# Kernel tuning notes

Hardware: AMD Instinct MI355X
Metric: run time of the kernel (lower is better)

Reference implementation:

```python
import jax, jax.numpy as jnp
import numpy as np

B, T, C, H = 2, 2048, 2048, 16
D = C // H  # head_dim = 128
SCALE = 1.0 / np.sqrt(D)


def setup_inputs() -> dict:
    key = jax.random.key(0)
    ks = jax.random.split(key, 9)
    x = jax.random.normal(ks[0], (B, T, C), dtype=jnp.float32)
    # additive causal mask [T, T]
    attn_mask = jnp.where(jnp.tril(jnp.ones((T, T), dtype=bool)), 0.0, -1e9).astype(jnp.float32)
    s_cc = 1.0 / np.sqrt(C)
    s_cd = 1.0 / np.sqrt(C)
    Wq = jax.random.normal(ks[1], (C, C), dtype=jnp.float32) * s_cc
    Wk = jax.random.normal(ks[2], (D, C), dtype=jnp.float32) * s_cd
    Wv = jax.random.normal(ks[3], (D, C), dtype=jnp.float32) * s_cd
    Wo = jax.random.normal(ks[4], (C, C), dtype=jnp.float32) * s_cc
    bq = jnp.zeros((C,), jnp.float32)
    bk = jnp.zeros((D,), jnp.float32)
    bv = jnp.zeros((D,), jnp.float32)
    bo = jnp.zeros((C,), jnp.float32)
    return {"x": x, "attn_mask": attn_mask, "Wq": Wq, "bq": bq, "Wk": Wk,
            "bk": bk, "Wv": Wv, "bv": bv, "Wo": Wo, "bo": bo}


def reference(x, attn_mask, Wq, bq, Wk, bk, Wv, bv, Wo, bo):
    # projections (torch Linear: x @ W.T + b)
    q = (x @ Wq.T + bq).reshape(B, T, H, D).transpose(0, 2, 1, 3)  # [B,H,T,D]
    k = x @ Wk.T + bk                                              # [B,T,D] single KV head
    v = x @ Wv.T + bv                                              # [B,T,D]
    # scores: broadcast shared K over all H query heads
    scores = jnp.einsum('bhtd,bsd->bhts', q, k) * SCALE            # [B,H,T,T]
    scores = scores + attn_mask  # [T,T] broadcasts over B,H
    attn = jax.nn.softmax(scores, axis=-1)
    out = jnp.einsum('bhts,bsd->bhtd', attn, v)                    # [B,H,T,D]
    out = out.transpose(0, 2, 1, 3).reshape(B, T, C)
    return out @ Wo.T + bo
```

## Files before the change

kernel.cpp:

```cpp
#include <hip/hip_runtime.h>
#include <stdint.h>

typedef unsigned short u16;
typedef __attribute__((ext_vector_type(8))) __bf16 bf16x8;
typedef __attribute__((ext_vector_type(4))) float f32x4;
typedef __attribute__((ext_vector_type(8))) u16 u16x8;

#define B_SZ 2
#define T_SZ 2048
#define C_SZ 2048
#define H_SZ 16
#define D_SZ 128
#define NQKV 2304
#define ATT_SCALE 0.08838834764831845f

typedef __attribute__((address_space(1))) void* as1_void_p;
typedef __attribute__((address_space(3))) void* as3_void_p;

__device__ __forceinline__ u16 f2b(float f) {
  union { float f; uint32_t u; } c; c.f = f;
  return (u16)((c.u + 0x7FFFu + ((c.u >> 16) & 1u)) >> 16);
}

__device__ __forceinline__ void gload_lds16(const u16* g, u16* l) {
  __builtin_amdgcn_global_load_lds((as1_void_p)g, (as3_void_p)l, 16, 0, 0);
}

__global__ __launch_bounds__(256) void cast_to_bf16(const float* __restrict__ in,
                                                    u16* __restrict__ out, int n) {
  int idx = (blockIdx.x * 256 + threadIdx.x) * 4;
  if (idx >= n) return;
  float4 f = *(const float4*)&in[idx];
  ushort4 o4;
  o4.x = f2b(f.x); o4.y = f2b(f.y); o4.z = f2b(f.z); o4.w = f2b(f.w);
  *(ushort4*)&out[idx] = o4;
}

__global__ __launch_bounds__(256) void build_bias(const float* __restrict__ bq,
                                                  const float* __restrict__ bk,
                                                  const float* __restrict__ bv,
                                                  float* __restrict__ out) {
  int i = blockIdx.x * 256 + threadIdx.x;
  if (i < C_SZ) out[i] = bq[i];
  else if (i < C_SZ + D_SZ) out[i] = bk[i - C_SZ];
  else if (i < NQKV) out[i] = bv[i - C_SZ - D_SZ];
}

template <typename OutT>
__global__ __launch_bounds__(256) void gemm_bt(const u16* __restrict__ A,
                                               const u16* __restrict__ Bm,
                                               const float* __restrict__ bias,
                                               OutT* __restrict__ C,
                                               int K, int ldc) {
  __shared__ u16 lsA[128 * 32];
  __shared__ u16 lsB[128 * 32];
  const int tid = threadIdx.x;
  const int lane = tid & 63;
  const int wave = tid >> 6;
  const int wr = wave >> 1, wc = wave & 1;
  const int l16 = lane & 15, lq = lane >> 4;
  const int brow = blockIdx.y * 128;
  const int bcol = blockIdx.x * 128;

  f32x4 acc[4][4] = {};

  for (int k0 = 0; k0 < K; k0 += 32) {
    __syncthreads();
#pragma unroll
    for (int i = 0; i < 2; i++) {
      const int woff = (i * 4 + wave) * 512;
      const int eoff = woff + lane * 8;
      const int r = eoff >> 5, c = eoff & 31;
      gload_lds16(A + (size_t)(brow + r) * K + k0 + c, &lsA[woff]);
      gload_lds16(Bm + (size_t)(bcol + r) * K + k0 + c, &lsB[woff]);
    }
    __syncthreads();

    bf16x8 af[4], bfr[4];
#pragma unroll
    for (int mi = 0; mi < 4; mi++)
      af[mi] = *(const bf16x8*)&lsA[(wr * 64 + mi * 16 + l16) * 32 + lq * 8];
#pragma unroll
    for (int ni = 0; ni < 4; ni++)
      bfr[ni] = *(const bf16x8*)&lsB[(wc * 64 + ni * 16 + l16) * 32 + lq * 8];
#pragma unroll
    for (int mi = 0; mi < 4; mi++)
#pragma unroll
      for (int ni = 0; ni < 4; ni++)
        acc[mi][ni] = __builtin_amdgcn_mfma_f32_16x16x32_bf16(af[mi], bfr[ni], acc[mi][ni], 0, 0, 0);
  }

#pragma unroll
  for (int mi = 0; mi < 4; mi++)
#pragma unroll
    for (int ni = 0; ni < 4; ni++) {
      const int col = bcol + wc * 64 + ni * 16 + l16;
      const float bb = bias ? bias[col] : 0.0f;
#pragma unroll
      for (int r = 0; r < 4; r++) {
        const int row = brow + wr * 64 + mi * 16 + lq * 4 + r;
        const float v = acc[mi][ni][r] + bb;
        if constexpr (sizeof(OutT) == 2) {
          ((u16*)C)[(size_t)row * ldc + col] = f2b(v);
        } else {
          ((float*)C)[(size_t)row * ldc + col] = v;
        }
      }
    }
}

__global__ __launch_bounds__(256) void transpose_v(const u16* __restrict__ qkv,
                                                   u16* __restrict__ vT) {
  __shared__ u16 tile[64 * 136];
  const int tid = threadIdx.x;
  const int t0 = blockIdx.x * 64;
  const int b = blockIdx.y;
#pragma unroll
  for (int i = 0; i < 4; i++) {
    int idx = (i * 256 + tid) * 8;
    int r = idx >> 7, c = idx & 127;
    u16x8 v = *(const u16x8*)&qkv[(size_t)(b * T_SZ + t0 + r) * NQKV + (C_SZ + D_SZ) + c];
    *(u16x8*)&tile[r * 136 + c] = v;
  }
  __syncthreads();
#pragma unroll
  for (int i = 0; i < 4; i++) {
    int idx = (i * 256 + tid) * 8;
    int d = idx >> 6, t = idx & 63;
    u16x8 v;
#pragma unroll
    for (int j = 0; j < 8; j++) v[j] = tile[(t + j) * 136 + d];
    *(u16x8*)&vT[(size_t)(b * D_SZ + d) * T_SZ + t0 + t] = v;
  }
}

__device__ __forceinline__ void attn_tile(
    const u16* lk, const u16* lv, u16* lsPw,
    const bf16x8 (&aq)[4], f32x4 (&o)[8], float (&mrow)[4], float (&lrow)[4],
    int relrow, int l16, int lq)
{
  f32x4 s[4] = {};
#pragma unroll
  for (int kk = 0; kk < 4; kk++) {
#pragma unroll
    for (int nb = 0; nb < 4; nb++) {
      const int row = nb * 16 + l16;
      const bf16x8 bk = *(const bf16x8*)&lk[row * 128 + (((kk * 4 + lq) ^ (row & 7)) << 3)];
      s[nb] = __builtin_amdgcn_mfma_f32_16x16x32_bf16(aq[kk], bk, s[nb], 0, 0, 0);
    }
  }
#pragma unroll
  for (int rr = 0; rr < 4; rr++) {
    const int rowrel = relrow + lq * 4 + rr;
    float mx = -3.0e38f;
#pragma unroll
    for (int nb = 0; nb < 4; nb++) {
      float xv = s[nb][rr] * ATT_SCALE;
      if (nb * 16 + l16 > rowrel) xv -= 1e9f;
      s[nb][rr] = xv;
      mx = fmaxf(mx, xv);
    }
#pragma unroll
    for (int sh = 8; sh >= 1; sh >>= 1) mx = fmaxf(mx, __shfl_xor(mx, sh, 64));
    const float mnew = fmaxf(mrow[rr], mx);
    const float alpha = __expf(mrow[rr] - mnew);
    mrow[rr] = mnew;
    float rs = 0.f;
#pragma unroll
    for (int nb = 0; nb < 4; nb++) {
      const float p = __expf(s[nb][rr] - mnew);
      s[nb][rr] = p;
      rs += p;
    }
#pragma unroll
    for (int sh = 8; sh >= 1; sh >>= 1) rs += __shfl_xor(rs, sh, 64);
    lrow[rr] = lrow[rr] * alpha + rs;
#pragma unroll
    for (int nd = 0; nd < 8; nd++) o[nd][rr] *= alpha;
  }
  __builtin_amdgcn_sched_barrier(0);
#pragma unroll
  for (int nb = 0; nb < 4; nb++)
#pragma unroll
    for (int rr = 0; rr < 4; rr++) {
      const int qr = lq * 4 + rr;
      const int col = nb * 16 + l16;
      lsPw[qr * 64 + ((((col >> 3) ^ (qr & 7)) << 3) | (col & 7))] = f2b(s[nb][rr]);
    }
  asm volatile("s_waitcnt lgkmcnt(0)" ::: "memory");
  __builtin_amdgcn_sched_barrier(0);
#pragma unroll
  for (int ks = 0; ks < 2; ks++) {
    const bf16x8 pa = *(const bf16x8*)&lsPw[l16 * 64 + (((ks * 4 + lq) ^ (l16 & 7)) << 3)];
#pragma unroll
    for (int nd = 0; nd < 8; nd++) {
      const int row = nd * 16 + l16;
      const bf16x8 bv = *(const bf16x8*)&lv[row * 64 + (((ks * 4 + lq) ^ (row & 7)) << 3)];
      o[nd] = __builtin_amdgcn_mfma_f32_16x16x32_bf16(pa, bv, o[nd], 0, 0, 0);
    }
  }
}

__global__ __launch_bounds__(256, 2) void attn_fwd(const u16* __restrict__ qkv,
                                                   const u16* __restrict__ vT,
                                                   u16* __restrict__ out) {
  __shared__ u16 lsK[2][64 * 128];
  __shared__ u16 lsV[2][128 * 64];
  __shared__ u16 lsP[4][16 * 64];
  const int tid = threadIdx.x;
  const int w = tid >> 6, lane = tid & 63;
  const int l16 = lane & 15, lq = lane >> 4;
  const int qL = blockIdx.x;
  const int qH = 31 - qL;
  const int h = blockIdx.y;
  const int b = blockIdx.z;
  const int bT = b * T_SZ;

  bf16x8 aqL[4], aqH[4];
  {
    const size_t rL = (size_t)(bT + qL * 64 + w * 16 + l16) * NQKV + h * D_SZ;
    const size_t rH = (size_t)(bT + qH * 64 + w * 16 + l16) * NQKV + h * D_SZ;
#pragma unroll
    for (int kk = 0; kk < 4; kk++) {
      aqL[kk] = *(const bf16x8*)&qkv[rL + kk * 32 + lq * 8];
      aqH[kk] = *(const bf16x8*)&qkv[rH + kk * 32 + lq * 8];
    }
  }

  f32x4 oL[8] = {}, oH[8] = {};
  float mL[4] = {-INFINITY, -INFINITY, -INFINITY, -INFINITY};
  float mH[4] = {-INFINITY, -INFINITY, -INFINITY, -INFINITY};
  float lL[4] = {0.f, 0.f, 0.f, 0.f};
  float lH[4] = {0.f, 0.f, 0.f, 0.f};

  auto STAGE = [&](int kt, int bufsel) {
    const int kv0 = kt << 6;
#pragma unroll
    for (int j = 0; j < 4; j++) {
      const int idx = w * 256 + j * 64 + lane;
      const int row = idx >> 4, c = idx & 15;
      const int sc = c ^ (row & 7);
      gload_lds16(qkv + (size_t)(bT + kv0 + row) * NQKV + C_SZ + sc * 8,
                  &lsK[bufsel][w * 2048 + j * 512]);
    }
#pragma unroll
    for (int j = 0; j < 4; j++) {
      const int idx = w * 256 + j * 64 + lane;
      const int row = idx >> 3, c = idx & 7;
      const int sc = c ^ (row & 7);
      gload_lds16(vT + (size_t)(b * D_SZ + row) * T_SZ + kv0 + sc * 8,
                  &lsV[bufsel][w * 2048 + j * 512]);
    }
  };

  STAGE(0, 0);
  __syncthreads();
  int cur = 0;
  for (int kt = 0; kt <= qH; kt++) {
    if (kt < qH) STAGE(kt + 1, cur ^ 1);
    attn_tile(lsK[cur], lsV[cur], lsP[w], aqH, oH, mH, lH,
              (qH - kt) * 64 + w * 16, l16, lq);
    if (kt <= qL)
      attn_tile(lsK[cur], lsV[cur], lsP[w], aqL, oL, mL, lL,
                (qL - kt) * 64 + w * 16, l16, lq);
    __syncthreads();
    cur ^= 1;
  }

#pragma unroll
  for (int nd = 0; nd < 8; nd++)
#pragma unroll
    for (int rr = 0; rr < 4; rr++) {
      const int rL_ = qL * 64 + w * 16 + lq * 4 + rr;
      const int rH_ = qH * 64 + w * 16 + lq * 4 + rr;
      out[(size_t)(bT + rL_) * C_SZ + h * D_SZ + nd * 16 + l16] = f2b(oL[nd][rr] / lL[rr]);
      out[(size_t)(bT + rH_) * C_SZ + h * D_SZ + nd * 16 + l16] = f2b(oH[nd][rr] / lH[rr]);
    }
}

extern "C" void kernel_launch(void* const* d_in, const int* in_sizes, int n_in,
                              void* d_out, int out_size, void* d_ws, size_t ws_size,
                              hipStream_t stream) {
  const float* x  = (const float*)d_in[0];
  const float* Wq = (const float*)d_in[2];
  const float* bq = (const float*)d_in[3];
  const float* Wk = (const float*)d_in[4];
  const float* bk = (const float*)d_in[5];
  const float* Wv = (const float*)d_in[6];
  const float* bv = (const float*)d_in[7];
  const float* Wo = (const float*)d_in[8];
  const float* bo = (const float*)d_in[9];
  float* out = (float*)d_out;

  char* ws = (char*)d_ws;
  if (ws_size < 71312384) return;
  u16* xb     = (u16*)(ws + 0);
  u16* wqkv   = (u16*)(ws + 16777216);
  u16* wob    = (u16*)(ws + 26214400);
  u16* qkv    = (u16*)(ws + 34603008);
  u16* vT     = (u16*)(ws + 53477376);
  u16* ao     = (u16*)(ws + 54525952);
  float* bqkv = (float*)(ws + 71303168);

  cast_to_bf16<<<8192, 256, 0, stream>>>(x, xb, 8388608);
  cast_to_bf16<<<4096, 256, 0, stream>>>(Wq, wqkv, 4194304);
  cast_to_bf16<<<256, 256, 0, stream>>>(Wk, wqkv + 4194304, 262144);
  cast_to_bf16<<<256, 256, 0, stream>>>(Wv, wqkv + 4456448, 262144);
  cast_to_bf16<<<4096, 256, 0, stream>>>(Wo, wob, 4194304);
  build_bias<<<9, 256, 0, stream>>>(bq, bk, bv, bqkv);

  gemm_bt<u16><<<dim3(18, 32), 256, 0, stream>>>(xb, wqkv, bqkv, qkv, 2048, NQKV);
  transpose_v<<<dim3(32, 2), 256, 0, stream>>>(qkv, vT);
  attn_fwd<<<dim3(16, 16, 2), 256, 0, stream>>>(qkv, vT, ao);
  gemm_bt<float><<<dim3(16, 32), 256, 0, stream>>>(ao, wob, bo, out, 2048, 2048);
}
```

Measured before the change: 245.5 us.

## Restructure attention into 32-key tiles with lazy softmax rescale and causal skipping

The attention kernel drops the paired low/high query-tile scheme and launches one block per 64-row query tile, heaviest first. K/V tiles shrink to 32 keys, so LDS use is smaller and occupancy can rise (launch bounds raised to 4 blocks per CU). Each warp skips key tiles entirely above its own 16 query rows and applies the causal mask only on diagonal tiles. Softmax now uses one running max per warp group that is updated only when it grows past a threshold (FA4-style deferred rescale), scale is folded into exp, and row-sum reductions move to the epilogue. The risks are more load imbalance without pairing, and precision issues from the shared, lagging max.

Result: slower. 277.9 us (+13.2%).

```diff
diff --git a/kernel.cpp b/kernel.cpp
--- a/kernel.cpp
+++ b/kernel.cpp
@@ -13,6 +13,7 @@
 #define D_SZ 128
 #define NQKV 2304
 #define ATT_SCALE 0.08838834764831845f
+#define DEFER_THR 90.50967f
 
 typedef __attribute__((address_space(1))) void* as1_void_p;
 typedef __attribute__((address_space(3))) void* as3_void_p;
@@ -134,147 +135,144 @@
   }
 }
 
-__device__ __forceinline__ void attn_tile(
+template <bool MASK>
+__device__ __forceinline__ void attn_tile32(
     const u16* lk, const u16* lv, u16* lsPw,
-    const bf16x8 (&aq)[4], f32x4 (&o)[8], float (&mrow)[4], float (&lrow)[4],
-    int relrow, int l16, int lq)
+    const bf16x8 (&aq)[4], f32x4 (&o)[8], float (&lp)[4], float& mgrp,
+    int relq, int l16, int lq)
 {
-  f32x4 s[4] = {};
+  f32x4 s[2] = {};
 #pragma unroll
   for (int kk = 0; kk < 4; kk++) {
 #pragma unroll
-    for (int nb = 0; nb < 4; nb++) {
+    for (int nb = 0; nb < 2; nb++) {
       const int row = nb * 16 + l16;
       const bf16x8 bk = *(const bf16x8*)&lk[row * 128 + (((kk * 4 + lq) ^ (row & 7)) << 3)];
       s[nb] = __builtin_amdgcn_mfma_f32_16x16x32_bf16(aq[kk], bk, s[nb], 0, 0, 0);
     }
   }
-#pragma unroll
-  for (int rr = 0; rr < 4; rr++) {
-    const int rowrel = relrow + lq * 4 + rr;
-    float mx = -3.0e38f;
-#pragma unroll
-    for (int nb = 0; nb < 4; nb++) {
-      float xv = s[nb][rr] * ATT_SCALE;
-      if (nb * 16 + l16 > rowrel) xv -= 1e9f;
-      s[nb][rr] = xv;
-      mx = fmaxf(mx, xv);
-    }
-#pragma unroll
-    for (int sh = 8; sh >= 1; sh >>= 1) mx = fmaxf(mx, __shfl_xor(mx, sh, 64));
-    const float mnew = fmaxf(mrow[rr], mx);
-    const float alpha = __expf(mrow[rr] - mnew);
-    mrow[rr] = mnew;
-    float rs = 0.f;
-#pragma unroll
-    for (int nb = 0; nb < 4; nb++) {
-      const float p = __expf(s[nb][rr] - mnew);
-      s[nb][rr] = p;
-      rs += p;
-    }
-#pragma unroll
-    for (int sh = 8; sh >= 1; sh >>= 1) rs += __shfl_xor(rs, sh, 64);
-    lrow[rr] = lrow[rr] * alpha + rs;
-#pragma unroll
-    for (int nd = 0; nd < 8; nd++) o[nd][rr] *= alpha;
-  }
-  __builtin_amdgcn_sched_barrier(0);
-#pragma unroll
-  for (int nb = 0; nb < 4; nb++)
+  if (MASK) {
+#pragma unroll
+    for (int nb = 0; nb < 2; nb++)
+#pragma unroll
+      for (int rr = 0; rr < 4; rr++)
+        if (nb * 16 + l16 > relq + rr) s[nb][rr] -= 1e9f;
+  }
+  float mx = fmaxf(fmaxf(fmaxf(s[0][0], s[0][1]), fmaxf(s[0][2], s[0][3])),
+                   fmaxf(fmaxf(s[1][0], s[1][1]), fmaxf(s[1][2], s[1][3])));
+#pragma unroll
+  for (int sh = 8; sh >= 1; sh >>= 1) mx = fmaxf(mx, __shfl_xor(mx, sh, 64));
+  if (__any(mx > mgrp + DEFER_THR)) {
+    const float mnew = fmaxf(mgrp, mx);
+    const float alpha = __expf((mgrp - mnew) * ATT_SCALE);
+    mgrp = mnew;
+#pragma unroll
+    for (int rr = 0; rr < 4; rr++) lp[rr] *= alpha;
+#pragma unroll
+    for (int nd = 0; nd < 8; nd++)
+#pragma unroll
+      for (int e = 0; e < 4; e++) o[nd][e] *= alpha;
+  }
+#pragma unroll
+  for (int nb = 0; nb < 2; nb++)
 #pragma unroll
     for (int rr = 0; rr < 4; rr++) {
+      const float p = __expf((s[nb][rr] - mgrp) * ATT_SCALE);
+      lp[rr] += p;
       const int qr = lq * 4 + rr;
       const int col = nb * 16 + l16;
-      lsPw[qr * 64 + ((((col >> 3) ^ (qr & 7)) << 3) | (col & 7))] = f2b(s[nb][rr]);
+      lsPw[qr * 32 + ((((col >> 3) ^ (qr & 3)) << 3) | (col & 7))] = f2b(p);
     }
   asm volatile("s_waitcnt lgkmcnt(0)" ::: "memory");
   __builtin_amdgcn_sched_barrier(0);
-#pragma unroll
-  for (int ks = 0; ks < 2; ks++) {
-    const bf16x8 pa = *(const bf16x8*)&lsPw[l16 * 64 + (((ks * 4 + lq) ^ (l16 & 7)) << 3)];
-#pragma unroll
-    for (int nd = 0; nd < 8; nd++) {
-      const int row = nd * 16 + l16;
-      const bf16x8 bv = *(const bf16x8*)&lv[row * 64 + (((ks * 4 + lq) ^ (row & 7)) << 3)];
-      o[nd] = __builtin_amdgcn_mfma_f32_16x16x32_bf16(pa, bv, o[nd], 0, 0, 0);
-    }
-  }
-}
-
-__global__ __launch_bounds__(256, 2) void attn_fwd(const u16* __restrict__ qkv,
+  const bf16x8 pa = *(const bf16x8*)&lsPw[l16 * 32 + ((lq ^ (l16 & 3)) << 3)];
+#pragma unroll
+  for (int nd = 0; nd < 8; nd++) {
+    const int row = nd * 16 + l16;
+    const bf16x8 bv = *(const bf16x8*)&lv[row * 32 + ((lq ^ (row & 3)) << 3)];
+    o[nd] = __builtin_amdgcn_mfma_f32_16x16x32_bf16(pa, bv, o[nd], 0, 0, 0);
+  }
+}
+
+__global__ __launch_bounds__(256, 4) void attn_fwd(const u16* __restrict__ qkv,
                                                    const u16* __restrict__ vT,
                                                    u16* __restrict__ out) {
-  __shared__ u16 lsK[2][64 * 128];
-  __shared__ u16 lsV[2][128 * 64];
-  __shared__ u16 lsP[4][16 * 64];
+  __shared__ u16 lsK[2][32 * 128];
+  __shared__ u16 lsV[2][128 * 32];
+  __shared__ u16 lsP[4][16 * 32];
   const int tid = threadIdx.x;
   const int w = tid >> 6, lane = tid & 63;
   const int l16 = lane & 15, lq = lane >> 4;
-  const int qL = blockIdx.x;
-  const int qH = 31 - qL;
+  const int qt = 31 - blockIdx.x;
   const int h = blockIdx.y;
   const int b = blockIdx.z;
   const int bT = b * T_SZ;
-
-  bf16x8 aqL[4], aqH[4];
+  const int wq0 = qt * 64 + w * 16;
+
+  bf16x8 aq[4];
   {
-    const size_t rL = (size_t)(bT + qL * 64 + w * 16 + l16) * NQKV + h * D_SZ;
-    const size_t rH = (size_t)(bT + qH * 64 + w * 16 + l16) * NQKV + h * D_SZ;
-#pragma unroll
-    for (int kk = 0; kk < 4; kk++) {
-      aqL[kk] = *(const bf16x8*)&qkv[rL + kk * 32 + lq * 8];
-      aqH[kk] = *(const bf16x8*)&qkv[rH + kk * 32 + lq * 8];
-    }
-  }
-
-  f32x4 oL[8] = {}, oH[8] = {};
-  float mL[4] = {-INFINITY, -INFINITY, -INFINITY, -INFINITY};
-  float mH[4] = {-INFINITY, -INFINITY, -INFINITY, -INFINITY};
-  float lL[4] = {0.f, 0.f, 0.f, 0.f};
-  float lH[4] = {0.f, 0.f, 0.f, 0.f};
+    const size_t qrow = (size_t)(bT + wq0 + l16) * NQKV + h * D_SZ;
+#pragma unroll
+    for (int kk = 0; kk < 4; kk++)
+      aq[kk] = *(const bf16x8*)&qkv[qrow + kk * 32 + lq * 8];
+  }
+
+  f32x4 o[8] = {};
+  float lp[4] = {0.f, 0.f, 0.f, 0.f};
+  float mgrp = -INFINITY;
 
   auto STAGE = [&](int kt, int bufsel) {
-    const int kv0 = kt << 6;
-#pragma unroll
-    for (int j = 0; j < 4; j++) {
-      const int idx = w * 256 + j * 64 + lane;
-      const int row = idx >> 4, c = idx & 15;
-      const int sc = c ^ (row & 7);
-      gload_lds16(qkv + (size_t)(bT + kv0 + row) * NQKV + C_SZ + sc * 8,
-                  &lsK[bufsel][w * 2048 + j * 512]);
-    }
-#pragma unroll
-    for (int j = 0; j < 4; j++) {
-      const int idx = w * 256 + j * 64 + lane;
-      const int row = idx >> 3, c = idx & 7;
-      const int sc = c ^ (row & 7);
-      gload_lds16(vT + (size_t)(b * D_SZ + row) * T_SZ + kv0 + sc * 8,
-                  &lsV[bufsel][w * 2048 + j * 512]);
+    const int kv0 = kt << 5;
+#pragma unroll
+    for (int j = 0; j < 2; j++) {
+      const int idx = w * 128 + j * 64 + lane;
+      {
+        const int row = idx >> 4, c = idx & 15;
+        const int sc = c ^ (row & 7);
+        gload_lds16(qkv + (size_t)(bT + kv0 + row) * NQKV + C_SZ + sc * 8,
+                    &lsK[bufsel][(w * 128 + j * 64) * 8]);
+      }
+      {
+        const int row = idx >> 2, c = idx & 3;
+        const int sc = c ^ (row & 3);
+        gload_lds16(vT + (size_t)(b * D_SZ + row) * T_SZ + kv0 + sc * 8,
+                    &lsV[bufsel][(w * 128 + j * 64) * 8]);
+      }
     }
   };
 
+  const int nkt = 2 * qt + 2;
   STAGE(0, 0);
   __syncthreads();
   int cur = 0;
-  for (int kt = 0; kt <= qH; kt++) {
-    if (kt < qH) STAGE(kt + 1, cur ^ 1);
-    attn_tile(lsK[cur], lsV[cur], lsP[w], aqH, oH, mH, lH,
-              (qH - kt) * 64 + w * 16, l16, lq);
-    if (kt <= qL)
-      attn_tile(lsK[cur], lsV[cur], lsP[w], aqL, oL, mL, lL,
-                (qL - kt) * 64 + w * 16, l16, lq);
+  for (int kt = 0; kt < nkt; kt++) {
+    const int kv0 = kt << 5;
+    if (kt + 1 < nkt) STAGE(kt + 1, cur ^ 1);
+    if (kv0 + 31 <= wq0) {
+      attn_tile32<false>(lsK[cur], lsV[cur], lsP[w], aq, o, lp, mgrp,
+                         0, l16, lq);
+    } else if (kv0 <= wq0 + 15) {
+      attn_tile32<true>(lsK[cur], lsV[cur], lsP[w], aq, o, lp, mgrp,
+                        wq0 - kv0 + lq * 4, l16, lq);
+    }
     __syncthreads();
     cur ^= 1;
   }
 
+  float lr[4];
+#pragma unroll
+  for (int rr = 0; rr < 4; rr++) {
+    float l = lp[rr];
+#pragma unroll
+    for (int sh = 8; sh >= 1; sh >>= 1) l += __shfl_xor(l, sh, 64);
+    lr[rr] = l;
+  }
 #pragma unroll
   for (int nd = 0; nd < 8; nd++)
 #pragma unroll
     for (int rr = 0; rr < 4; rr++) {
-      const int rL_ = qL * 64 + w * 16 + lq * 4 + rr;
-      const int rH_ = qH * 64 + w * 16 + lq * 4 + rr;
-      out[(size_t)(bT + rL_) * C_SZ + h * D_SZ + nd * 16 + l16] = f2b(oL[nd][rr] / lL[rr]);
-      out[(size_t)(bT + rH_) * C_SZ + h * D_SZ + nd * 16 + l16] = f2b(oH[nd][rr] / lH[rr]);
+      const int row = wq0 + lq * 4 + rr;
+      out[(size_t)(bT + row) * C_SZ + h * D_SZ + nd * 16 + l16] = f2b(o[nd][rr] / lr[rr]);
     }
 }
 
@@ -311,6 +309,6 @@
 
   gemm_bt<u16><<<dim3(18, 32), 256, 0, stream>>>(xb, wqkv, bqkv, qkv, 2048, NQKV);
   transpose_v<<<dim3(32, 2), 256, 0, stream>>>(qkv, vT);
-  attn_fwd<<<dim3(16, 16, 2), 256, 0, stream>>>(qkv, vT, ao);
+  attn_fwd<<<dim3(32, 16, 2), 256, 0, stream>>>(qkv, vT, ao);
   gemm_bt<float><<<dim3(16, 32), 256, 0, stream>>>(ao, wob, bo, out, 2048, 2048);
 }
```

## Defer softmax rescaling, specialize diagonal mask, double-buffer GEMM LDS

Applied to the files above, without the earlier changes.

The attention inner loop now keeps a single running max per wave, which is approximately per group of rows. It rescales the output accumulators only when a new max exceeds the old one by a threshold, and it folds scale and log2e into exp2f. Row sums are accumulated per lane and reduced once at the end, causal masking is compiled only into the diagonal tile, and the final normalization uses a reciprocal instead of a divide. The projection GEMM gains double-buffered LDS staging so the next K-slice loads overlap the MFMAs. The deferred-max scheme risks overflow or precision loss if scores grow past the threshold margin.

After: 225.1 us. 8.3% less time.

```diff
diff --git a/kernel.cpp b/kernel.cpp
--- a/kernel.cpp
+++ b/kernel.cpp
@@ -13,6 +13,8 @@
 #define D_SZ 128
 #define NQKV 2304
 #define ATT_SCALE 0.08838834764831845f
+#define LOG2E_SCALE 0.12751744f
+#define DEFER_THR 90.50967f
 
 typedef __attribute__((address_space(1))) void* as1_void_p;
 typedef __attribute__((address_space(3))) void* as3_void_p;
@@ -52,8 +54,8 @@
                                                const float* __restrict__ bias,
                                                OutT* __restrict__ C,
                                                int K, int ldc) {
-  __shared__ u16 lsA[128 * 32];
-  __shared__ u16 lsB[128 * 32];
+  __shared__ u16 lsA[2][128 * 32];
+  __shared__ u16 lsB[2][128 * 32];
   const int tid = threadIdx.x;
   const int lane = tid & 63;
   const int wave = tid >> 6;
@@ -64,30 +66,38 @@
 
   f32x4 acc[4][4] = {};
 
-  for (int k0 = 0; k0 < K; k0 += 32) {
-    __syncthreads();
+  auto STAGE = [&](int k0, int bs) {
 #pragma unroll
     for (int i = 0; i < 2; i++) {
       const int woff = (i * 4 + wave) * 512;
       const int eoff = woff + lane * 8;
       const int r = eoff >> 5, c = eoff & 31;
-      gload_lds16(A + (size_t)(brow + r) * K + k0 + c, &lsA[woff]);
-      gload_lds16(Bm + (size_t)(bcol + r) * K + k0 + c, &lsB[woff]);
-    }
-    __syncthreads();
+      gload_lds16(A + (size_t)(brow + r) * K + k0 + c, &lsA[bs][woff]);
+      gload_lds16(Bm + (size_t)(bcol + r) * K + k0 + c, &lsB[bs][woff]);
+    }
+  };
+
+  STAGE(0, 0);
+  __syncthreads();
+  int cur = 0;
+  for (int k0 = 0; k0 < K; k0 += 32) {
+    if (k0 + 32 < K) STAGE(k0 + 32, cur ^ 1);
 
     bf16x8 af[4], bfr[4];
 #pragma unroll
     for (int mi = 0; mi < 4; mi++)
-      af[mi] = *(const bf16x8*)&lsA[(wr * 64 + mi * 16 + l16) * 32 + lq * 8];
+      af[mi] = *(const bf16x8*)&lsA[cur][(wr * 64 + mi * 16 + l16) * 32 + lq * 8];
 #pragma unroll
     for (int ni = 0; ni < 4; ni++)
-      bfr[ni] = *(const bf16x8*)&lsB[(wc * 64 + ni * 16 + l16) * 32 + lq * 8];
+      bfr[ni] = *(const bf16x8*)&lsB[cur][(wc * 64 + ni * 16 + l16) * 32 + lq * 8];
 #pragma unroll
     for (int mi = 0; mi < 4; mi++)
 #pragma unroll
       for (int ni = 0; ni < 4; ni++)
         acc[mi][ni] = __builtin_amdgcn_mfma_f32_16x16x32_bf16(af[mi], bfr[ni], acc[mi][ni], 0, 0, 0);
+
+    __syncthreads();
+    cur ^= 1;
   }
 
 #pragma unroll
@@ -134,10 +144,11 @@
   }
 }
 
-__device__ __forceinline__ void attn_tile(
+template <bool MASK>
+__device__ __forceinline__ void attn_tile64(
     const u16* lk, const u16* lv, u16* lsPw,
-    const bf16x8 (&aq)[4], f32x4 (&o)[8], float (&mrow)[4], float (&lrow)[4],
-    int relrow, int l16, int lq)
+    const bf16x8 (&aq)[4], f32x4 (&o)[8], float (&lp)[4], float& mgrp,
+    int relq, int l16, int lq)
 {
   f32x4 s[4] = {};
 #pragma unroll
@@ -149,43 +160,40 @@
       s[nb] = __builtin_amdgcn_mfma_f32_16x16x32_bf16(aq[kk], bk, s[nb], 0, 0, 0);
     }
   }
-#pragma unroll
-  for (int rr = 0; rr < 4; rr++) {
-    const int rowrel = relrow + lq * 4 + rr;
-    float mx = -3.0e38f;
-#pragma unroll
-    for (int nb = 0; nb < 4; nb++) {
-      float xv = s[nb][rr] * ATT_SCALE;
-      if (nb * 16 + l16 > rowrel) xv -= 1e9f;
-      s[nb][rr] = xv;
-      mx = fmaxf(mx, xv);
-    }
-#pragma unroll
-    for (int sh = 8; sh >= 1; sh >>= 1) mx = fmaxf(mx, __shfl_xor(mx, sh, 64));
-    const float mnew = fmaxf(mrow[rr], mx);
-    const float alpha = __expf(mrow[rr] - mnew);
-    mrow[rr] = mnew;
-    float rs = 0.f;
-#pragma unroll
-    for (int nb = 0; nb < 4; nb++) {
-      const float p = __expf(s[nb][rr] - mnew);
-      s[nb][rr] = p;
-      rs += p;
-    }
-#pragma unroll
-    for (int sh = 8; sh >= 1; sh >>= 1) rs += __shfl_xor(rs, sh, 64);
-    lrow[rr] = lrow[rr] * alpha + rs;
-#pragma unroll
-    for (int nd = 0; nd < 8; nd++) o[nd][rr] *= alpha;
-  }
-  __builtin_amdgcn_sched_barrier(0);
+  if (MASK) {
+#pragma unroll
+    for (int nb = 0; nb < 4; nb++)
+#pragma unroll
+      for (int rr = 0; rr < 4; rr++)
+        if (nb * 16 + l16 > relq + rr) s[nb][rr] -= 1e9f;
+  }
+  float mx = s[0][0];
 #pragma unroll
   for (int nb = 0; nb < 4; nb++)
 #pragma unroll
+    for (int rr = 0; rr < 4; rr++) mx = fmaxf(mx, s[nb][rr]);
+#pragma unroll
+  for (int sh = 8; sh >= 1; sh >>= 1) mx = fmaxf(mx, __shfl_xor(mx, sh, 64));
+  if (__any(mx > mgrp + DEFER_THR)) {
+    const float mnew = fmaxf(mgrp, mx);
+    const float alpha = exp2f((mgrp - mnew) * LOG2E_SCALE);
+    mgrp = mnew;
+#pragma unroll
+    for (int rr = 0; rr < 4; rr++) lp[rr] *= alpha;
+#pragma unroll
+    for (int nd = 0; nd < 8; nd++)
+#pragma unroll
+      for (int e = 0; e < 4; e++) o[nd][e] *= alpha;
+  }
+#pragma unroll
+  for (int nb = 0; nb < 4; nb++)
+#pragma unroll
     for (int rr = 0; rr < 4; rr++) {
+      const float p = exp2f((s[nb][rr] - mgrp) * LOG2E_SCALE);
+      lp[rr] += p;
       const int qr = lq * 4 + rr;
       const int col = nb * 16 + l16;
-      lsPw[qr * 64 + ((((col >> 3) ^ (qr & 7)) << 3) | (col & 7))] = f2b(s[nb][rr]);
+      lsPw[qr * 64 + ((((col >> 3) ^ (qr & 7)) << 3) | (col & 7))] = f2b(p);
     }
   asm volatile("s_waitcnt lgkmcnt(0)" ::: "memory");
   __builtin_amdgcn_sched_barrier(0);
@@ -228,10 +236,10 @@
   }
 
   f32x4 oL[8] = {}, oH[8] = {};
-  float mL[4] = {-INFINITY, -INFINITY, -INFINITY, -INFINITY};
-  float mH[4] = {-INFINITY, -INFINITY, -INFINITY, -INFINITY};
-  float lL[4] = {0.f, 0.f, 0.f, 0.f};
-  float lH[4] = {0.f, 0.f, 0.f, 0.f};
+  float lpL[4] = {0.f, 0.f, 0.f, 0.f};
+  float lpH[4] = {0.f, 0.f, 0.f, 0.f};
+  float mL = -INFINITY, mH = -INFINITY;
+  const int relDiag = w * 16 + lq * 4;
 
   auto STAGE = [&](int kt, int bufsel) {
     const int kv0 = kt << 6;
@@ -258,23 +266,38 @@
   int cur = 0;
   for (int kt = 0; kt <= qH; kt++) {
     if (kt < qH) STAGE(kt + 1, cur ^ 1);
-    attn_tile(lsK[cur], lsV[cur], lsP[w], aqH, oH, mH, lH,
-              (qH - kt) * 64 + w * 16, l16, lq);
-    if (kt <= qL)
-      attn_tile(lsK[cur], lsV[cur], lsP[w], aqL, oL, mL, lL,
-                (qL - kt) * 64 + w * 16, l16, lq);
+    if (kt == qH)
+      attn_tile64<true>(lsK[cur], lsV[cur], lsP[w], aqH, oH, lpH, mH, relDiag, l16, lq);
+    else
+      attn_tile64<false>(lsK[cur], lsV[cur], lsP[w], aqH, oH, lpH, mH, 0, l16, lq);
+    if (kt == qL)
+      attn_tile64<true>(lsK[cur], lsV[cur], lsP[w], aqL, oL, lpL, mL, relDiag, l16, lq);
+    else if (kt < qL)
+      attn_tile64<false>(lsK[cur], lsV[cur], lsP[w], aqL, oL, lpL, mL, 0, l16, lq);
     __syncthreads();
     cur ^= 1;
   }
 
+  float rL4[4], rH4[4];
+#pragma unroll
+  for (int rr = 0; rr < 4; rr++) {
+    float a = lpL[rr], c = lpH[rr];
+#pragma unroll
+    for (int sh = 8; sh >= 1; sh >>= 1) {
+      a += __shfl_xor(a, sh, 64);
+      c += __shfl_xor(c, sh, 64);
+    }
+    rL4[rr] = __builtin_amdgcn_rcpf(a);
+    rH4[rr] = __builtin_amdgcn_rcpf(c);
+  }
 #pragma unroll
   for (int nd = 0; nd < 8; nd++)
 #pragma unroll
     for (int rr = 0; rr < 4; rr++) {
       const int rL_ = qL * 64 + w * 16 + lq * 4 + rr;
       const int rH_ = qH * 64 + w * 16 + lq * 4 + rr;
-      out[(size_t)(bT + rL_) * C_SZ + h * D_SZ + nd * 16 + l16] = f2b(oL[nd][rr] / lL[rr]);
-      out[(size_t)(bT + rH_) * C_SZ + h * D_SZ + nd * 16 + l16] = f2b(oH[nd][rr] / lH[rr]);
+      out[(size_t)(bT + rL_) * C_SZ + h * D_SZ + nd * 16 + l16] = f2b(oL[nd][rr] * rL4[rr]);
+      out[(size_t)(bT + rH_) * C_SZ + h * D_SZ + nd * 16 + l16] = f2b(oH[nd][rr] * rH4[rr]);
     }
 }
 
```
